# Performance work log

Measured on AMD Instinct MI355X. Metric: run time of the kernel, lower is better.

Reference implementation:

```python
import jax, jax.numpy as jnp
import numpy as np

DEGREE = 2
STEPS = 7
N_FEATURES = 120
R_TARGETS = 4
LATENT = 4
D = N_FEATURES + R_TARGETS + LATENT          # 128: padded state dim
N_POLY = 1 + D + D * D                       # 16513: sum_{k=0..degree} D^k for degree=2
BATCH = 16384
W_SCALE = 1e-4                               # keep the iterated quadratic map stable


def setup_inputs() -> dict:
    key = jax.random.key(0)
    k1, k2 = jax.random.split(key)
    X = jax.random.normal(k1, (BATCH, N_FEATURES), dtype=jnp.float32)
    W = jax.random.normal(k2, (N_POLY, D), dtype=jnp.float32) * W_SCALE
    t_init = jnp.zeros((R_TARGETS,), dtype=jnp.float32)
    l_init = jnp.zeros((LATENT,), dtype=jnp.float32)
    return {"X": X, "W": W, "t_init": t_init, "l_init": l_init}


def _poly_full(x):
    """PolynomialFeatures via repeated outer products: [1, x, vec(x xp_{k-1}^T), ...]."""
    n = x.shape[0]
    xp = [jnp.ones((n, 1), x.dtype), x]
    for _ in range(2, DEGREE + 1):
        # [n, D, 1] * [n, 1, P] -> [n, D*P]  (matches tf: X @ expand_dims(XP[-1],1))
        xp.append((x[:, :, None] * xp[-1][:, None, :]).reshape(n, -1))
    return jnp.concatenate(xp, axis=-1)  # [n, N_POLY]


def reference(X, W, t_init, l_init):
    # pad inputs with r_targets + latent_units zeros, then add init values
    inits = jnp.concatenate([jnp.zeros((N_FEATURES,), X.dtype), t_init, l_init])
    x0 = jnp.pad(X, ((0, 0), (0, R_TARGETS + LATENT))) + inits  # [B, D]

    def step(x, _):
        return x + _poly_full(x) @ W, None  # TaylorMap: residual + poly GEMM

    x, _ = jax.lax.scan(step, x0, None, length=STEPS)
    # self._targets = target_features + appended extra target dims
    return x[:, N_FEATURES:N_FEATURES + R_TARGETS]  # [B, n_targets]
```

## Files before the change

### kernel.cpp

```cpp
#include <hip/hip_runtime.h>
#include <hip/hip_bf16.h>


#define DSTATE 128
#define BATCH  16384
#define NSTEPS 7
#define BT     64
#define NSL    585

typedef __attribute__((ext_vector_type(8)))  short  short8;
typedef __attribute__((ext_vector_type(16))) float  f32x16;

__device__ __forceinline__ unsigned short f2bf(float f){
    unsigned int u = __float_as_uint(f);
    u += 0x7fff + ((u >> 16) & 1);
    return (unsigned short)(u >> 16);
}

__global__ void prep_kernel(const float* __restrict__ W, short8* __restrict__ A){
    int gid = blockIdx.x * 256 + threadIdx.x;
    const int ntotal = 4 * 130 * 8 * 64;
    if (gid >= ntotal) return;
    int lane = gid & 63; int r = gid >> 6;
    int s = r & 7;  r >>= 3;
    int row = r % 130;
    int t   = r / 130;
    int d  = t * 32 + (lane & 31);
    int kb = (lane >> 5) * 8;
    int dst;
    bool zero = false;
    if (row < 64){
        int sl = row >> 4;
        if (s < sl) return;
        dst = t * NSL + 9 * row + (s - sl);
    } else if (row < 128){
        int p  = 127 - row;
        int sl = row >> 4;
        if (s < sl) return;
        int ca = 8 - (p >> 4);
        dst = t * NSL + 9 * p + ca + (s - sl);
    } else if (row == 128){
        dst = t * NSL + 576 + s;
    } else {
        if (s) return;
        dst = t * NSL + 584;
        zero = true;
    }
    union { short8 v; unsigned short u[8]; } fr;
#pragma unroll
    for (int e = 0; e < 8; ++e){
        int j = s * 16 + kb + e;
        float v;
        if (zero) v = 0.0f;
        else if (row < 128){
            if      (j < row)  v = 0.0f;
            else if (j == row) v = W[(129 + 128 * row + j) * 128 + d];
            else               v = W[(129 + 128 * row + j) * 128 + d]
                                 + W[(129 + 128 * j + row) * 128 + d];
        } else {
            v = W[(1 + j) * 128 + d];
        }
        fr.u[e] = f2bf(v);
    }
    A[(size_t)dst * 64 + lane] = fr.v;
}

__global__ __launch_bounds__(512)
void taylor_kernel(const float* __restrict__ X, const float* __restrict__ W,
                   const float* __restrict__ tini, const float* __restrict__ lini,
                   const short8* __restrict__ A, float* __restrict__ out)
{
    __shared__ float  x_lds[DSTATE * BT];
    __shared__ float  w0_lds[DSTATE];
    __shared__ short8 bpack[2 * 8 * 64];
    __shared__ float  sc_lds[2][4 * 64 * 17];

    const int tid  = threadIdx.x;
    const int lane = tid & 63;
    const int w    = tid >> 6;
    const int t    = w & 3;
    const int g    = w >> 2;
    const int ln   = lane & 31;
    const int hi   = lane >> 5;
    const int b0   = blockIdx.x * BT;

#pragma unroll
    for (int it = 0; it < 16; ++it){
        int entry = tid + it * 512;
        int b = entry >> 7, d = entry & 127;
        float v;
        if      (d < 120) v = X[(b0 + b) * 120 + d];
        else if (d < 124) v = tini[d - 120];
        else              v = lini[d - 124];
        x_lds[d * BT + b] = v;
    }
    if (tid < DSTATE) w0_lds[tid] = W[tid];

    const short8* const Aw = A + ((size_t)t * NSL + (size_t)g * 288) * 64 + lane;
    const f32x16 zero16 = {};

#pragma unroll 1
    for (int step = 0; step < NSTEPS; ++step){
        __syncthreads();

        const short8* ap = Aw;
        short8 abuf[9];
#pragma unroll
        for (int s = 0; s < 9; ++s) abuf[s] = ap[s * 64];
        ap += 9 * 64;

#pragma unroll
        for (int f0 = 0; f0 < 2; ++f0){
            int f  = tid + f0 * 512;
            int gg = f >> 9, s = (f >> 6) & 7, l = f & 63;
            int c  = gg * 32 + (l & 31);
            int jb = 16 * s + 8 * (l >> 5);
            union { short8 v; unsigned short u[8]; } fr;
#pragma unroll
            for (int e = 0; e < 8; ++e)
                fr.u[e] = f2bf(x_lds[(jb + e) * BT + c]);
            bpack[f] = fr.v;
        }

        f32x16 acc0, acc1;
        if (g == 0){
#pragma unroll
            for (int r = 0; r < 16; ++r){
                int d = 32 * t + (r & 3) + 8 * (r >> 2) + 4 * hi;
                acc0[r] = x_lds[d * BT + ln]      + w0_lds[d];
                acc1[r] = x_lds[d * BT + 32 + ln] + w0_lds[d];
            }
        } else {
#pragma unroll
            for (int r = 0; r < 16; ++r){ acc0[r] = 0.f; acc1[r] = 0.f; }
        }

        __syncthreads();

        short8 bfrag0[8], bfrag1[8];

#define PAIRS(BK)                                                               \
        {                                                                       \
            _Pragma("unroll")                                                   \
            for (int s = 0; s < 8 - (BK); ++s){                                 \
                bfrag0[s] = bpack[((BK) + s) * 64 + lane];                      \
                bfrag1[s] = bpack[512 + ((BK) + s) * 64 + lane];                \
            }                                                                   \
            _Pragma("unroll 2")                                                 \
            for (int q = 0; q < 16; ++q){                                       \
                const int p = 16 * (BK) + q;                                    \
                float s0a = x_lds[p * BT + ln];                                 \
                float s0b = x_lds[p * BT + 32 + ln];                            \
                float s1a = x_lds[(127 - p) * BT + ln];                         \
                float s1b = x_lds[(127 - p) * BT + 32 + ln];                    \
                f32x16 Y0, Y1;                                                  \
                _Pragma("unroll")                                               \
                for (int s = 0; s < 8 - (BK); ++s){                             \
                    Y0 = __builtin_amdgcn_mfma_f32_32x32x16_bf16(abuf[s], bfrag0[s], s ? Y0 : zero16, 0, 0, 0); \
                    Y1 = __builtin_amdgcn_mfma_f32_32x32x16_bf16(abuf[s], bfrag1[s], s ? Y1 : zero16, 0, 0, 0); \
                    abuf[s] = ap[s * 64];                                       \
                }                                                               \
                acc0 += s0a * Y0;                                               \
                acc1 += s0b * Y1;                                               \
                f32x16 Z0, Z1;                                                  \
                _Pragma("unroll")                                               \
                for (int s = 0; s < 1 + (BK); ++s){                             \
                    Z0 = __builtin_amdgcn_mfma_f32_32x32x16_bf16(abuf[8 - (BK) + s], bfrag0[7 - 2 * (BK) + s], s ? Z0 : zero16, 0, 0, 0); \
                    Z1 = __builtin_amdgcn_mfma_f32_32x32x16_bf16(abuf[8 - (BK) + s], bfrag1[7 - 2 * (BK) + s], s ? Z1 : zero16, 0, 0, 0); \
                    abuf[8 - (BK) + s] = ap[(8 - (BK) + s) * 64];               \
                }                                                               \
                acc0 += s1a * Z0;                                               \
                acc1 += s1b * Z1;                                               \
                ap += 9 * 64;                                                   \
            }                                                                   \
        }

        if (g == 0){
            PAIRS(0) PAIRS(1)
        } else {
            PAIRS(2) PAIRS(3)
            f32x16 Y0, Y1;
#pragma unroll
            for (int s = 0; s < 8; ++s){
                bfrag0[s] = bpack[s * 64 + lane];
                bfrag1[s] = bpack[512 + s * 64 + lane];
            }
#pragma unroll
            for (int s = 0; s < 8; ++s){
                Y0 = __builtin_amdgcn_mfma_f32_32x32x16_bf16(abuf[s], bfrag0[s], s ? Y0 : zero16, 0, 0, 0);
                Y1 = __builtin_amdgcn_mfma_f32_32x32x16_bf16(abuf[s], bfrag1[s], s ? Y1 : zero16, 0, 0, 0);
            }
            acc0 += Y0;
            acc1 += Y1;
#pragma unroll
            for (int r = 0; r < 16; ++r){
                sc_lds[0][(t * 64 + lane) * 17 + r] = acc0[r];
                sc_lds[1][(t * 64 + lane) * 17 + r] = acc1[r];
            }
        }
#undef PAIRS

        __syncthreads();
        if (g == 0){
#pragma unroll
            for (int r = 0; r < 16; ++r){
                acc0[r] += sc_lds[0][(t * 64 + lane) * 17 + r];
                acc1[r] += sc_lds[1][(t * 64 + lane) * 17 + r];
            }
            if (step < NSTEPS - 1){
#pragma unroll
                for (int r = 0; r < 16; ++r){
                    int d = 32 * t + (r & 3) + 8 * (r >> 2) + 4 * hi;
                    x_lds[d * BT + ln]      = acc0[r];
                    x_lds[d * BT + 32 + ln] = acc1[r];
                }
            } else if (t == 3 && hi == 0){
                *(float4*)(out + (size_t)(b0 + ln) * 4) =
                    make_float4(acc0[12], acc0[13], acc0[14], acc0[15]);
                *(float4*)(out + (size_t)(b0 + 32 + ln) * 4) =
                    make_float4(acc1[12], acc1[13], acc1[14], acc1[15]);
            }
        }
    }
}

extern "C" void kernel_launch(void* const* d_in, const int* in_sizes, int n_in,
                              void* d_out, int out_size, void* d_ws, size_t ws_size,
                              hipStream_t stream)
{
    const float* X  = (const float*)d_in[0];
    const float* W  = (const float*)d_in[1];
    const float* ti = (const float*)d_in[2];
    const float* li = (const float*)d_in[3];
    float* out      = (float*)d_out;
    short8* A       = (short8*)d_ws;

    const int ntotal = 4 * 130 * 8 * 64;
    prep_kernel<<<(ntotal + 255) / 256, 256, 0, stream>>>(W, A);
    taylor_kernel<<<BATCH / BT, 512, 0, stream>>>(X, W, ti, li, A, out);
}
```

Baseline: 325.1 us.

## Fold per-row scale into fp16 B operand and accumulate directly in MFMA

Switches the MFMA path from bf16 to fp16, scaling the weights by 256 in prep and the state by 1/256 to keep values in fp16 range. The per-pair scalar x_p is multiplied into the B fragment with packed half multiplies, so the MFMAs accumulate straight into acc0/acc1. This removes the temporary Y/Z accumulators and the 16-wide fp32 scale-and-add after each chain. The cost is extra packed fp16 multiplies per MFMA and tighter fp16 precision and range limits on the scaled products.

After: 352.4 us. +8.4%, slower.

```diff
diff --git a/kernel.cpp b/kernel.cpp
--- a/kernel.cpp
+++ b/kernel.cpp
@@ -7,17 +7,18 @@
 #define NSTEPS 7
 #define BT     64
 #define NSL    585
-
-typedef __attribute__((ext_vector_type(8)))  short  short8;
-typedef __attribute__((ext_vector_type(16))) float  f32x16;
-
-__device__ __forceinline__ unsigned short f2bf(float f){
-    unsigned int u = __float_as_uint(f);
-    u += 0x7fff + ((u >> 16) & 1);
-    return (unsigned short)(u >> 16);
-}
-
-__global__ void prep_kernel(const float* __restrict__ W, short8* __restrict__ A){
+#define ASCALE 256.0f
+#define INVAS  0.00390625f
+
+typedef __attribute__((ext_vector_type(8)))  _Float16 half8;
+typedef __attribute__((ext_vector_type(16))) float    f32x16;
+
+__device__ __forceinline__ half8 splat8(_Float16 h){
+    half8 v = {h, h, h, h, h, h, h, h};
+    return v;
+}
+
+__global__ void prep_kernel(const float* __restrict__ W, half8* __restrict__ A){
     int gid = blockIdx.x * 256 + threadIdx.x;
     const int ntotal = 4 * 130 * 8 * 64;
     if (gid >= ntotal) return;
@@ -46,7 +47,7 @@
         dst = t * NSL + 584;
         zero = true;
     }
-    union { short8 v; unsigned short u[8]; } fr;
+    union { half8 v; _Float16 u[8]; } fr;
 #pragma unroll
     for (int e = 0; e < 8; ++e){
         int j = s * 16 + kb + e;
@@ -60,7 +61,7 @@
         } else {
             v = W[(1 + j) * 128 + d];
         }
-        fr.u[e] = f2bf(v);
+        fr.u[e] = (_Float16)(v * ASCALE);
     }
     A[(size_t)dst * 64 + lane] = fr.v;
 }
@@ -68,11 +69,11 @@
 __global__ __launch_bounds__(512)
 void taylor_kernel(const float* __restrict__ X, const float* __restrict__ W,
                    const float* __restrict__ tini, const float* __restrict__ lini,
-                   const short8* __restrict__ A, float* __restrict__ out)
+                   const half8* __restrict__ A, float* __restrict__ out)
 {
     __shared__ float  x_lds[DSTATE * BT];
     __shared__ float  w0_lds[DSTATE];
-    __shared__ short8 bpack[2 * 8 * 64];
+    __shared__ half8  bpack[2 * 8 * 64];
     __shared__ float  sc_lds[2][4 * 64 * 17];
 
     const int tid  = threadIdx.x;
@@ -96,15 +97,14 @@
     }
     if (tid < DSTATE) w0_lds[tid] = W[tid];
 
-    const short8* const Aw = A + ((size_t)t * NSL + (size_t)g * 288) * 64 + lane;
-    const f32x16 zero16 = {};
+    const half8* const Aw = A + ((size_t)t * NSL + (size_t)g * 288) * 64 + lane;
 
 #pragma unroll 1
     for (int step = 0; step < NSTEPS; ++step){
         __syncthreads();
 
-        const short8* ap = Aw;
-        short8 abuf[9];
+        const half8* ap = Aw;
+        half8 abuf[9];
 #pragma unroll
         for (int s = 0; s < 9; ++s) abuf[s] = ap[s * 64];
         ap += 9 * 64;
@@ -115,10 +115,10 @@
             int gg = f >> 9, s = (f >> 6) & 7, l = f & 63;
             int c  = gg * 32 + (l & 31);
             int jb = 16 * s + 8 * (l >> 5);
-            union { short8 v; unsigned short u[8]; } fr;
+            union { half8 v; _Float16 u[8]; } fr;
 #pragma unroll
             for (int e = 0; e < 8; ++e)
-                fr.u[e] = f2bf(x_lds[(jb + e) * BT + c]);
+                fr.u[e] = (_Float16)x_lds[(jb + e) * BT + c];
             bpack[f] = fr.v;
         }
 
@@ -137,7 +137,7 @@
 
         __syncthreads();
 
-        short8 bfrag0[8], bfrag1[8];
+        half8 bfrag0[8], bfrag1[8];
 
 #define PAIRS(BK)                                                               \
         {                                                                       \
@@ -149,28 +149,22 @@
             _Pragma("unroll 2")                                                 \
             for (int q = 0; q < 16; ++q){                                       \
                 const int p = 16 * (BK) + q;                                    \
-                float s0a = x_lds[p * BT + ln];                                 \
-                float s0b = x_lds[p * BT + 32 + ln];                            \
-                float s1a = x_lds[(127 - p) * BT + ln];                         \
-                float s1b = x_lds[(127 - p) * BT + 32 + ln];                    \
-                f32x16 Y0, Y1;                                                  \
+                half8 v0a = splat8((_Float16)(x_lds[p * BT + ln]            * INVAS)); \
+                half8 v0b = splat8((_Float16)(x_lds[p * BT + 32 + ln]       * INVAS)); \
+                half8 v1a = splat8((_Float16)(x_lds[(127 - p) * BT + ln]      * INVAS)); \
+                half8 v1b = splat8((_Float16)(x_lds[(127 - p) * BT + 32 + ln] * INVAS)); \
                 _Pragma("unroll")                                               \
                 for (int s = 0; s < 8 - (BK); ++s){                             \
-                    Y0 = __builtin_amdgcn_mfma_f32_32x32x16_bf16(abuf[s], bfrag0[s], s ? Y0 : zero16, 0, 0, 0); \
-                    Y1 = __builtin_amdgcn_mfma_f32_32x32x16_bf16(abuf[s], bfrag1[s], s ? Y1 : zero16, 0, 0, 0); \
+                    acc0 = __builtin_amdgcn_mfma_f32_32x32x16_f16(abuf[s], v0a * bfrag0[s], acc0, 0, 0, 0); \
+                    acc1 = __builtin_amdgcn_mfma_f32_32x32x16_f16(abuf[s], v0b * bfrag1[s], acc1, 0, 0, 0); \
                     abuf[s] = ap[s * 64];                                       \
                 }                                                               \
-                acc0 += s0a * Y0;                                               \
-                acc1 += s0b * Y1;                                               \
-                f32x16 Z0, Z1;                                                  \
                 _Pragma("unroll")                                               \
                 for (int s = 0; s < 1 + (BK); ++s){                             \
-                    Z0 = __builtin_amdgcn_mfma_f32_32x32x16_bf16(abuf[8 - (BK) + s], bfrag0[7 - 2 * (BK) + s], s ? Z0 : zero16, 0, 0, 0); \
-                    Z1 = __builtin_amdgcn_mfma_f32_32x32x16_bf16(abuf[8 - (BK) + s], bfrag1[7 - 2 * (BK) + s], s ? Z1 : zero16, 0, 0, 0); \
+                    acc0 = __builtin_amdgcn_mfma_f32_32x32x16_f16(abuf[8 - (BK) + s], v1a * bfrag0[7 - 2 * (BK) + s], acc0, 0, 0, 0); \
+                    acc1 = __builtin_amdgcn_mfma_f32_32x32x16_f16(abuf[8 - (BK) + s], v1b * bfrag1[7 - 2 * (BK) + s], acc1, 0, 0, 0); \
                     abuf[8 - (BK) + s] = ap[(8 - (BK) + s) * 64];               \
                 }                                                               \
-                acc0 += s1a * Z0;                                               \
-                acc1 += s1b * Z1;                                               \
                 ap += 9 * 64;                                                   \
             }                                                                   \
         }
@@ -179,7 +173,7 @@
             PAIRS(0) PAIRS(1)
         } else {
             PAIRS(2) PAIRS(3)
-            f32x16 Y0, Y1;
+            const half8 vlin = splat8((_Float16)INVAS);
 #pragma unroll
             for (int s = 0; s < 8; ++s){
                 bfrag0[s] = bpack[s * 64 + lane];
@@ -187,11 +181,9 @@
             }
 #pragma unroll
             for (int s = 0; s < 8; ++s){
-                Y0 = __builtin_amdgcn_mfma_f32_32x32x16_bf16(abuf[s], bfrag0[s], s ? Y0 : zero16, 0, 0, 0);
-                Y1 = __builtin_amdgcn_mfma_f32_32x32x16_bf16(abuf[s], bfrag1[s], s ? Y1 : zero16, 0, 0, 0);
-            }
-            acc0 += Y0;
-            acc1 += Y1;
+                acc0 = __builtin_amdgcn_mfma_f32_32x32x16_f16(abuf[s], vlin * bfrag0[s], acc0, 0, 0, 0);
+                acc1 = __builtin_amdgcn_mfma_f32_32x32x16_f16(abuf[s], vlin * bfrag1[s], acc1, 0, 0, 0);
+            }
 #pragma unroll
             for (int r = 0; r < 16; ++r){
                 sc_lds[0][(t * 64 + lane) * 17 + r] = acc0[r];
@@ -233,7 +225,7 @@
     const float* ti = (const float*)d_in[2];
     const float* li = (const float*)d_in[3];
     float* out      = (float*)d_out;
-    short8* A       = (short8*)d_ws;
+    half8* A        = (half8*)d_ws;
 
     const int ntotal = 4 * 130 * 8 * 64;
     prep_kernel<<<(ntotal + 255) / 256, 256, 0, stream>>>(W, A);
```

## Skip non-target output tiles on final step and software-pipeline Y/Z MFMA chains

Applied to the files above, without the earlier changes.

On the last iteration only the output tile holding the target dims (t==3) does GEMM work. The other wave groups skip the A-fragment loads and all MFMAs, because their results are never written. The inner loop is also software-pipelined: the Y chain for the next pair is issued after the Z chain, and its scaled accumulate is deferred one iteration, so MFMA latency can overlap with LDS loads and FMAs. The final linear-term MFMAs now accumulate directly into acc instead of going through a temporary. These changes add register pressure and code complexity. The skip cuts about 1/7 of the work for three quarters of the waves.

Result: slower. 332.8 us (+2.4%).

```diff
diff --git a/kernel.cpp b/kernel.cpp
--- a/kernel.cpp
+++ b/kernel.cpp
@@ -103,11 +103,15 @@
     for (int step = 0; step < NSTEPS; ++step){
         __syncthreads();
 
+        const bool active = (step < NSTEPS - 1) || (t == 3);
+
         const short8* ap = Aw;
         short8 abuf[9];
-#pragma unroll
-        for (int s = 0; s < 9; ++s) abuf[s] = ap[s * 64];
-        ap += 9 * 64;
+        if (active){
+#pragma unroll
+            for (int s = 0; s < 9; ++s) abuf[s] = ap[s * 64];
+            ap += 9 * 64;
+        }
 
 #pragma unroll
         for (int f0 = 0; f0 < 2; ++f0){
@@ -123,45 +127,28 @@
         }
 
         f32x16 acc0, acc1;
-        if (g == 0){
-#pragma unroll
-            for (int r = 0; r < 16; ++r){
-                int d = 32 * t + (r & 3) + 8 * (r >> 2) + 4 * hi;
-                acc0[r] = x_lds[d * BT + ln]      + w0_lds[d];
-                acc1[r] = x_lds[d * BT + 32 + ln] + w0_lds[d];
-            }
-        } else {
-#pragma unroll
-            for (int r = 0; r < 16; ++r){ acc0[r] = 0.f; acc1[r] = 0.f; }
+        if (active){
+            if (g == 0){
+#pragma unroll
+                for (int r = 0; r < 16; ++r){
+                    int d = 32 * t + (r & 3) + 8 * (r >> 2) + 4 * hi;
+                    acc0[r] = x_lds[d * BT + ln]      + w0_lds[d];
+                    acc1[r] = x_lds[d * BT + 32 + ln] + w0_lds[d];
+                }
+            } else {
+#pragma unroll
+                for (int r = 0; r < 16; ++r){ acc0[r] = 0.f; acc1[r] = 0.f; }
+            }
         }
 
         __syncthreads();
 
-        short8 bfrag0[8], bfrag1[8];
-
-#define PAIRS(BK)                                                               \
-        {                                                                       \
-            _Pragma("unroll")                                                   \
-            for (int s = 0; s < 8 - (BK); ++s){                                 \
-                bfrag0[s] = bpack[((BK) + s) * 64 + lane];                      \
-                bfrag1[s] = bpack[512 + ((BK) + s) * 64 + lane];                \
-            }                                                                   \
-            _Pragma("unroll 2")                                                 \
-            for (int q = 0; q < 16; ++q){                                       \
-                const int p = 16 * (BK) + q;                                    \
-                float s0a = x_lds[p * BT + ln];                                 \
-                float s0b = x_lds[p * BT + 32 + ln];                            \
-                float s1a = x_lds[(127 - p) * BT + ln];                         \
-                float s1b = x_lds[(127 - p) * BT + 32 + ln];                    \
-                f32x16 Y0, Y1;                                                  \
-                _Pragma("unroll")                                               \
-                for (int s = 0; s < 8 - (BK); ++s){                             \
-                    Y0 = __builtin_amdgcn_mfma_f32_32x32x16_bf16(abuf[s], bfrag0[s], s ? Y0 : zero16, 0, 0, 0); \
-                    Y1 = __builtin_amdgcn_mfma_f32_32x32x16_bf16(abuf[s], bfrag1[s], s ? Y1 : zero16, 0, 0, 0); \
-                    abuf[s] = ap[s * 64];                                       \
-                }                                                               \
-                acc0 += s0a * Y0;                                               \
-                acc1 += s0b * Y1;                                               \
+        if (active){
+            short8 bfrag0[8], bfrag1[8];
+            f32x16 Yp0, Yp1;
+            float  cs0a, cs0b;
+
+#define ZYCORE(BK)                                                              \
                 f32x16 Z0, Z1;                                                  \
                 _Pragma("unroll")                                               \
                 for (int s = 0; s < 1 + (BK); ++s){                             \
@@ -169,39 +156,81 @@
                     Z1 = __builtin_amdgcn_mfma_f32_32x32x16_bf16(abuf[8 - (BK) + s], bfrag1[7 - 2 * (BK) + s], s ? Z1 : zero16, 0, 0, 0); \
                     abuf[8 - (BK) + s] = ap[(8 - (BK) + s) * 64];               \
                 }                                                               \
+                _Pragma("unroll")                                               \
+                for (int s = 0; s < 8 - (BK); ++s){                             \
+                    Yp0 = __builtin_amdgcn_mfma_f32_32x32x16_bf16(abuf[s], bfrag0[s], s ? Yp0 : zero16, 0, 0, 0); \
+                    Yp1 = __builtin_amdgcn_mfma_f32_32x32x16_bf16(abuf[s], bfrag1[s], s ? Yp1 : zero16, 0, 0, 0); \
+                    abuf[s] = ap[s * 64];                                       \
+                }                                                               \
+                ap += 9 * 64;
+
+#define BLOAD(BK)                                                               \
+            _Pragma("unroll")                                                   \
+            for (int s = 0; s < 8 - (BK); ++s){                                 \
+                bfrag0[s] = bpack[((BK) + s) * 64 + lane];                      \
+                bfrag1[s] = bpack[512 + ((BK) + s) * 64 + lane];                \
+            }
+
+#define PROLOG(BK, P)                                                           \
+            BLOAD(BK)                                                           \
+            {                                                                   \
+                cs0a = x_lds[(P) * BT + ln];                                    \
+                cs0b = x_lds[(P) * BT + 32 + ln];                               \
+                float s1a = x_lds[(127 - (P)) * BT + ln];                       \
+                float s1b = x_lds[(127 - (P)) * BT + 32 + ln];                  \
+                ZYCORE(BK)                                                      \
                 acc0 += s1a * Z0;                                               \
                 acc1 += s1b * Z1;                                               \
-                ap += 9 * 64;                                                   \
-            }                                                                   \
-        }
-
-        if (g == 0){
-            PAIRS(0) PAIRS(1)
-        } else {
-            PAIRS(2) PAIRS(3)
-            f32x16 Y0, Y1;
-#pragma unroll
-            for (int s = 0; s < 8; ++s){
-                bfrag0[s] = bpack[s * 64 + lane];
-                bfrag1[s] = bpack[512 + s * 64 + lane];
-            }
-#pragma unroll
-            for (int s = 0; s < 8; ++s){
-                Y0 = __builtin_amdgcn_mfma_f32_32x32x16_bf16(abuf[s], bfrag0[s], s ? Y0 : zero16, 0, 0, 0);
-                Y1 = __builtin_amdgcn_mfma_f32_32x32x16_bf16(abuf[s], bfrag1[s], s ? Y1 : zero16, 0, 0, 0);
-            }
-            acc0 += Y0;
-            acc1 += Y1;
-#pragma unroll
-            for (int r = 0; r < 16; ++r){
-                sc_lds[0][(t * 64 + lane) * 17 + r] = acc0[r];
-                sc_lds[1][(t * 64 + lane) * 17 + r] = acc1[r];
-            }
-        }
+            }
+
+#define PAIRS(BK, QA, QB)                                                       \
+            BLOAD(BK)                                                           \
+            _Pragma("unroll 2")                                                 \
+            for (int q = (QA); q < (QB); ++q){                                  \
+                const int p = 16 * (BK) + q;                                    \
+                acc0 += cs0a * Yp0;                \
+                acc1 += cs0b * Yp1;                                             \
+                cs0a = x_lds[p * BT + ln];                                      \
+                cs0b = x_lds[p * BT + 32 + ln];                                 \
+                float s1a = x_lds[(127 - p) * BT + ln];                         \
+                float s1b = x_lds[(127 - p) * BT + 32 + ln];                    \
+                ZYCORE(BK)                                                      \
+                acc0 += s1a * Z0;                                               \
+                acc1 += s1b * Z1;                                               \
+            }
+
+            if (g == 0){
+                PROLOG(0, 0)
+                PAIRS(0, 1, 16)
+                PAIRS(1, 0, 16)
+                acc0 += cs0a * Yp0;
+                acc1 += cs0b * Yp1;
+            } else {
+                PROLOG(2, 32)
+                PAIRS(2, 1, 16)
+                PAIRS(3, 0, 16)
+                acc0 += cs0a * Yp0;
+                acc1 += cs0b * Yp1;
+                BLOAD(0)
+#pragma unroll
+                for (int s = 0; s < 8; ++s){
+                    acc0 = __builtin_amdgcn_mfma_f32_32x32x16_bf16(abuf[s], bfrag0[s], acc0, 0, 0, 0);
+                    acc1 = __builtin_amdgcn_mfma_f32_32x32x16_bf16(abuf[s], bfrag1[s], acc1, 0, 0, 0);
+                }
+#pragma unroll
+                for (int r = 0; r < 16; ++r){
+                    sc_lds[0][(t * 64 + lane) * 17 + r] = acc0[r];
+                    sc_lds[1][(t * 64 + lane) * 17 + r] = acc1[r];
+                }
+            }
 #undef PAIRS
+#undef PROLOG
+#undef BLOAD
+#undef ZYCORE
+        }
 
         __syncthreads();
-        if (g == 0){
+        if (active && g == 0){
 #pragma unroll
             for (int r = 0; r < 16; ++r){
                 acc0[r] += sc_lds[0][(t * 64 + lane) * 17 + r];
@@ -214,11 +243,13 @@
                     x_lds[d * BT + ln]      = acc0[r];
                     x_lds[d * BT + 32 + ln] = acc1[r];
                 }
-            } else if (t == 3 && hi == 0){
-                *(float4*)(out + (size_t)(b0 + ln) * 4) =
-                    make_float4(acc0[12], acc0[13], acc0[14], acc0[15]);
-                *(float4*)(out + (size_t)(b0 + 32 + ln) * 4) =
-                    make_float4(acc1[12], acc1[13], acc1[14], acc1[15]);
+            } else {
+                if (hi == 0){
+                    *(float4*)(out + (size_t)(b0 + ln) * 4) =
+                        make_float4(acc0[12], acc0[13], acc0[14], acc0[15]);
+                    *(float4*)(out + (size_t)(b0 + 32 + ln) * 4) =
+                        make_float4(acc1[12], acc1[13], acc1[14], acc1[15]);
+                }
             }
         }
     }
```
